# Kernel tuning notes

Hardware: AMD Instinct MI355X
Metric: run time of the kernel (lower is better)

The kernel has to match this reference:

```python
import jax, jax.numpy as jnp
import numpy as np

BS, N, HID, INPUT, PREK, KHOP = 16, 1024, 64, 64, 4, 3
D = 2 * HID            # hidden channel dim (128)
F = 2 * INPUT          # input feature dim (128)
C = F + D              # graphconv input channels (256)
NM = KHOP + 1          # num_metrics = k_hop*n_supports + 1 with n_supports=1
PI = 3.141592653589793
EMB_RANGE = (12.0 + 2.0) / HID   # (gamma + epsilon) / hidden_size


def setup_inputs() -> dict:
    key = jax.random.key(0)
    ks = jax.random.split(key, 12)
    inputs = jax.random.normal(ks[0], (BS, N, F), jnp.float32)
    # per-sample dynamic support; scale by 1/N to keep Chebyshev recursion stable
    supports = jax.random.uniform(ks[1], (BS, N, N), jnp.float32) / N
    hidden_states = jax.random.normal(ks[2], (BS, PREK, N, D), jnp.float32)
    W = jax.random.normal(ks[3], (D, D), jnp.float32) * 0.02
    b = jax.random.normal(ks[4], (N, D), jnp.float32) * 0.02
    R = jax.random.normal(ks[5], (PREK, N, HID), jnp.float32) * 0.02
    gc_w = jax.random.normal(ks[6], (D, C * NM), jnp.float32) * 0.02
    gc_b = jax.random.normal(ks[7], (D,), jnp.float32) * 0.02
    ev_att_w = jax.random.normal(ks[8], (1, N * D), jnp.float32) * 0.001
    ev_att_b = jax.random.normal(ks[9], (1,), jnp.float32) * 0.02
    att_w = jax.random.normal(ks[10], (1, N * D), jnp.float32) * 0.001
    att_b = jax.random.normal(ks[11], (1,), jnp.float32) * 0.02
    return {"inputs": inputs, "supports": supports, "hidden_states": hidden_states,
            "W": W, "b": b, "R": R, "gc_w": gc_w, "gc_b": gc_b,
            "ev_att_w": ev_att_w, "ev_att_b": ev_att_b,
            "att_w": att_w, "att_b": att_b}


def reference(inputs, supports, hidden_states, W, b, R, gc_w, gc_b,
              ev_att_w, ev_att_b, att_w, att_b):
    bs, k, n, d = hidden_states.shape
    # split inputs / last hidden into real/imag halves
    re_in, im_in = jnp.split(inputs, 2, axis=-1)          # [bs,n,INPUT]
    preH = hidden_states[:, -1]                           # [bs,n,d]
    re_p, im_p = jnp.split(preH, 2, axis=-1)              # [bs,n,HID]
    conv_in = jnp.concatenate([re_in, re_p, im_in, im_p], axis=-1)  # [bs,n,C]

    # diffusion graph conv (Chebyshev-style recursion over single batched support)
    x0 = conv_in
    x1 = jnp.matmul(supports, x0)                         # [bs,n,C]
    xs = [x0, x1]
    for _ in range(2, KHOP + 1):
        x2 = 2.0 * jnp.matmul(supports, x1) - x0
        xs.append(x2)
        x0, x1 = x1, x2
    # stack K metrics, permute to [bs,n,C,K], flatten (channel-major, step-minor)
    x = jnp.stack(xs, axis=0).transpose(1, 2, 3, 0).reshape(bs, n, C * NM)
    gco = x @ gc_w.T + gc_b                               # [bs,n,d]

    # EvolutionCell attention over g=1 group (kept for faithfulness)
    xe = gco.reshape(bs, 1, n * d)
    se = xe @ ev_att_w.T + ev_att_b                       # [bs,1,1]
    we = jax.nn.softmax(se, axis=1)
    conv_out = (xe * we).sum(axis=1).reshape(bs, n, d)

    # leaky_relu_ (slope 0.01)
    conv_out = jnp.where(conv_out >= 0, conv_out, 0.01 * conv_out)

    # RotatE-style complex phase rotation of hidden states
    phase = R / (EMB_RANGE / PI)                          # [k,n,HID]
    re_rel, im_rel = jnp.cos(phase), jnp.sin(phase)
    re_h, im_h = jnp.split(hidden_states, 2, axis=-1)     # [bs,k,n,HID]
    re_new = re_rel * re_h - im_rel * im_h
    im_new = im_rel * re_h + re_rel * im_h
    new_states = jnp.concatenate([re_new, im_new], axis=-1)  # [bs,k,n,d]

    # attention over k memory slots
    xa = new_states.reshape(bs, k, n * d)
    sa = xa @ att_w.T + att_b                             # [bs,k,1]
    wa = jax.nn.softmax(sa, axis=1)
    att = (xa * wa).sum(axis=1).reshape(bs, n, d)

    output = conv_out @ W + b[None] + att                 # [bs,n,d]
    new_hidden = jnp.concatenate([hidden_states[:, 1:], output[:, None]], axis=1)
    return output, new_hidden
```

## Files before the change

### kernel.cpp

```cpp
#include <hip/hip_runtime.h>
#include <cstddef>

constexpr float PHASE_SCALE = (float)(3.141592653589793 / ((12.0 + 2.0) / 64.0));

typedef __bf16 bf16;
typedef __bf16 bf16x4 __attribute__((ext_vector_type(4)));
typedef __bf16 bf16x8 __attribute__((ext_vector_type(8)));
typedef float floatx4 __attribute__((ext_vector_type(4)));

#define GLOAD_LDS16(gp, lp) __builtin_amdgcn_global_load_lds( \
    (const __attribute__((address_space(1))) void*)(gp),      \
    (__attribute__((address_space(3))) void*)(lp), 16, 0, 0)

__global__ __launch_bounds__(256) void prep_kernel(
    const float4* __restrict__ S, bf16* __restrict__ Sbf,
    const float* __restrict__ R,
    const float* __restrict__ gcw, const float* __restrict__ W,
    bf16* __restrict__ gtAll, bf16* __restrict__ WT,
    const float* __restrict__ inp, const float* __restrict__ hs,
    bf16* __restrict__ xRow, bf16* __restrict__ xT0,
    const float* __restrict__ attw, float* __restrict__ part)
{
    __shared__ bf16 tile[64][65];
    __shared__ float red[256];
    const int bid = blockIdx.x;
    const int tid = threadIdx.x;

    if (bid < 512) {
        int bk = bid & 63;
        int k = bk & 3;
        int chunk = bid >> 6;
        const float* hbase = hs + (size_t)bk * 131072;
        float acc = 0.f;
        for (int idx = tid; idx < 2048; idx += 256) {
            int h4 = (idx & 15) * 4;
            int n = chunk * 128 + (idx >> 4);
            float4 rr  = *(const float4*)(R + (size_t)k * 65536 + n * 64 + h4);
            float4 re  = *(const float4*)(hbase + (size_t)n * 128 + h4);
            float4 im  = *(const float4*)(hbase + (size_t)n * 128 + 64 + h4);
            float4 wre = *(const float4*)(attw + (size_t)n * 128 + h4);
            float4 wim = *(const float4*)(attw + (size_t)n * 128 + 64 + h4);
            float sv, cv;
            __sincosf(rr.x * PHASE_SCALE, &sv, &cv);
            acc += (cv * re.x - sv * im.x) * wre.x + (sv * re.x + cv * im.x) * wim.x;
            __sincosf(rr.y * PHASE_SCALE, &sv, &cv);
            acc += (cv * re.y - sv * im.y) * wre.y + (sv * re.y + cv * im.y) * wim.y;
            __sincosf(rr.z * PHASE_SCALE, &sv, &cv);
            acc += (cv * re.z - sv * im.z) * wre.z + (sv * re.z + cv * im.z) * wim.z;
            __sincosf(rr.w * PHASE_SCALE, &sv, &cv);
            acc += (cv * re.w - sv * im.w) * wre.w + (sv * re.w + cv * im.w) * wim.w;
        }
        red[tid] = acc;
        __syncthreads();
        for (int s2 = 128; s2 > 0; s2 >>= 1) {
            if (tid < s2) red[tid] += red[tid + s2];
            __syncthreads();
        }
        if (tid == 0) part[bk * 8 + chunk] = red[0];
    } else if (bid < 1536) {
        int lin = bid - 512;
        int b = lin >> 6, by = (lin >> 2) & 15, bx = lin & 3;
        int n0 = by * 64, c0 = bx * 64;
        const float* base = (bx & 1) ? (hs + (((size_t)b * 4 + 3) * 1024) * 128)
                                     : (inp + ((size_t)b * 1024) * 128);
        int soff = (bx >> 1) * 64;
        #pragma unroll
        for (int it = 0; it < 2; ++it) {
            int unit = it * 256 + tid;
            int nl = unit >> 3, cs = unit & 7;
            const float* src = base + (size_t)(n0 + nl) * 128 + soff + cs * 8;
            float4 a0 = *(const float4*)src;
            float4 a1 = *(const float4*)(src + 4);
            bf16x8 o;
            o[0] = (bf16)a0.x; o[1] = (bf16)a0.y; o[2] = (bf16)a0.z; o[3] = (bf16)a0.w;
            o[4] = (bf16)a1.x; o[5] = (bf16)a1.y; o[6] = (bf16)a1.z; o[7] = (bf16)a1.w;
            *(bf16x8*)(xRow + ((size_t)b * 1024 + n0 + nl) * 256 + c0 + cs * 8) = o;
            #pragma unroll
            for (int e = 0; e < 8; ++e) tile[nl][cs * 8 + e] = o[e];
        }
        __syncthreads();
        #pragma unroll
        for (int it = 0; it < 4; ++it) {
            int unit = it * 256 + tid;
            int ng = unit & 15, cc = unit >> 4;
            bf16x4 v;
            #pragma unroll
            for (int r = 0; r < 4; ++r) v[r] = tile[ng * 4 + r][cc];
            *(bf16x4*)(xT0 + ((size_t)b * 256 + c0 + cc) * 1024 + n0 + ng * 4) = v;
        }
    } else if (bid < 2112) {
        int gi = (bid - 1536) * 256 + tid;
        if (gi < 131072) {
            int m = gi >> 15;
            int rem = gi & 32767;
            int d = rem >> 8;
            int c = rem & 255;
            gtAll[gi] = (bf16)gcw[(size_t)d * 1024 + c * 4 + m];
        } else {
            int r = gi - 131072;
            int n = r >> 7, k = r & 127;
            WT[r] = (bf16)W[(size_t)k * 128 + n];
        }
    } else {
        size_t u = (size_t)(bid - 2112) * 512;
        #pragma unroll
        for (int i = 0; i < 2; ++i) {
            size_t gi = u + i * 256 + tid;
            const float4* Sp = S + gi * 2;
            float4 v0 = Sp[0];
            float4 v1 = Sp[1];
            bf16x8 o;
            o[0] = (bf16)v0.x; o[1] = (bf16)v0.y; o[2] = (bf16)v0.z; o[3] = (bf16)v0.w;
            o[4] = (bf16)v1.x; o[5] = (bf16)v1.y; o[6] = (bf16)v1.z; o[7] = (bf16)v1.w;
            *(bf16x8*)(Sbf + gi * 8) = o;
        }
    }
}

__global__ __launch_bounds__(512) void cheb_mfma_kernel(
    const bf16* __restrict__ S, const bf16* __restrict__ xT,
    const bf16* __restrict__ xTprev, bf16* __restrict__ outT,
    const bf16* __restrict__ xRow0, const bf16* __restrict__ gtA,
    const bf16* __restrict__ gt0, float* __restrict__ gcoF,
    float alpha, int accumulate)
{
    __shared__ char smem[81920];
    const int f = blockIdx.x;
    const int b = (f & 7) + 8 * ((f >> 3) & 1);
    const int n0 = (f >> 4) * 64;
    const int tid = threadIdx.x;
    const int wave = tid >> 6, lane = tid & 63;
    const int wr = (wave & 3) * 16;
    const int wc = (wave >> 2) * 128;
    const int l15 = lane & 15, quad = lane >> 4;
    const int lrow = lane >> 3;
    const int segsw = (lane & 7) ^ lrow;

    const bf16* Sb = S + (size_t)b * 1048576;
    const bf16* xb = xT + (size_t)b * 262144;

    auto stage = [&](int p, int k0) {
        bf16* dA = (bf16*)(smem + p * 40960);
        bf16* dB = dA + 4096;
        {
            const bf16* gp = Sb + (size_t)(n0 + wave * 8 + lrow) * 1024 + k0 + segsw * 8;
            GLOAD_LDS16(gp, dA + wave * 8 * 64);
        }
        #pragma unroll
        for (int v = 0; v < 4; ++v) {
            int cq = wave * 32 + v * 8;
            const bf16* gp = xb + (size_t)(cq + lrow) * 1024 + k0 + segsw * 8;
            GLOAD_LDS16(gp, dB + cq * 64);
        }
    };

    floatx4 acc[8] = {};
    stage(0, 0);
    int p = 0;
    for (int k0 = 0; k0 < 1024; k0 += 64) {
        __syncthreads();
        if (k0 + 64 < 1024) stage(p ^ 1, k0 + 64);
        const bf16* lA = (const bf16*)(smem + p * 40960);
        const bf16* lB = lA + 4096;
        #pragma unroll
        for (int ks = 0; ks < 2; ++ks) {
            int row = wr + l15;
            int aslot = (ks * 4 + quad) ^ (row & 7);
            bf16x8 af = *(const bf16x8*)(lA + row * 64 + aslot * 8);
            #pragma unroll
            for (int j = 0; j < 8; ++j) {
                int col = wc + j * 16 + l15;
                int bslot = (ks * 4 + quad) ^ (col & 7);
                bf16x8 bfr = *(const bf16x8*)(lB + col * 64 + bslot * 8);
                acc[j] = __builtin_amdgcn_mfma_f32_16x16x32_bf16(af, bfr, acc[j], 0, 0, 0);
            }
        }
        p ^= 1;
    }

    const bf16* pT = xTprev ? xTprev + (size_t)b * 262144 : nullptr;
    bf16* oT = outT ? outT + (size_t)b * 262144 : nullptr;
    bf16x4 xo[8];
    #pragma unroll
    for (int j = 0; j < 8; ++j) {
        int col = wc + j * 16 + l15;
        float v[4];
        #pragma unroll
        for (int r = 0; r < 4; ++r) v[r] = alpha * acc[j][r];
        if (pT) {
            bf16x4 pp = *(const bf16x4*)(pT + (size_t)col * 1024 + n0 + wr + quad * 4);
            #pragma unroll
            for (int r = 0; r < 4; ++r) v[r] -= (float)pp[r];
        }
        #pragma unroll
        for (int r = 0; r < 4; ++r) xo[j][r] = (bf16)v[r];
        if (oT) *(bf16x4*)(oT + (size_t)col * 1024 + n0 + wr + quad * 4) = xo[j];
    }

    __syncthreads();
    bf16* ldsX = (bf16*)smem;
    #pragma unroll
    for (int j = 0; j < 8; ++j) {
        int col = wc + j * 16 + l15;
        #pragma unroll
        for (int r = 0; r < 4; ++r)
            ldsX[(wr + quad * 4 + r) * 264 + col] = xo[j][r];
    }
    __syncthreads();

    const int dbase = (wave >> 2) * 64;
    floatx4 a2[4] = {};
    for (int k2 = 0; k2 < 256; k2 += 32) {
        bf16x8 af = *(const bf16x8*)(ldsX + (wr + l15) * 264 + k2 + quad * 8);
        #pragma unroll
        for (int j = 0; j < 4; ++j) {
            int dcol = dbase + j * 16 + l15;
            bf16x8 bfr = *(const bf16x8*)(gtA + (size_t)dcol * 256 + k2 + quad * 8);
            a2[j] = __builtin_amdgcn_mfma_f32_16x16x32_bf16(af, bfr, a2[j], 0, 0, 0);
        }
    }
    if (xRow0) {
        for (int k2 = 0; k2 < 256; k2 += 32) {
            bf16x8 af = *(const bf16x8*)(xRow0 + ((size_t)b * 1024 + n0 + wr + l15) * 256 + k2 + quad * 8);
            #pragma unroll
            for (int j = 0; j < 4; ++j) {
                int dcol = dbase + j * 16 + l15;
                bf16x8 bfr = *(const bf16x8*)(gt0 + (size_t)dcol * 256 + k2 + quad * 8);
                a2[j] = __builtin_amdgcn_mfma_f32_16x16x32_bf16(af, bfr, a2[j], 0, 0, 0);
            }
        }
    }
    #pragma unroll
    for (int j = 0; j < 4; ++j) {
        int dcol = dbase + j * 16 + l15;
        #pragma unroll
        for (int r = 0; r < 4; ++r) {
            size_t idx = ((size_t)b * 1024 + n0 + wr + quad * 4 + r) * 128 + dcol;
            if (accumulate) gcoF[idx] += a2[j][r];
            else            gcoF[idx]  = a2[j][r];
        }
    }
}

__global__ __launch_bounds__(256) void final_kernel(
    const float* __restrict__ gcoF, const float* __restrict__ gcb,
    const bf16* __restrict__ WT, const float* __restrict__ bvec,
    const float* __restrict__ hs, const float* __restrict__ R,
    const float* __restrict__ part, const float* __restrict__ attb,
    float* __restrict__ out, float* __restrict__ newh)
{
    const int m0 = blockIdx.x * 64;
    const int b = m0 >> 10, n0 = m0 & 1023;
    const int tid = threadIdx.x;
    const int wave = tid >> 6, lane = tid & 63;
    const int l15 = lane & 15, quad = lane >> 4;

    const int arow = m0 + wave * 16 + l15;
    floatx4 acc[8] = {};
    #pragma unroll
    for (int k0 = 0; k0 < 128; k0 += 32) {
        int kk = k0 + quad * 8;
        float4 p0 = *(const float4*)(gcoF + (size_t)arow * 128 + kk);
        float4 p1 = *(const float4*)(gcoF + (size_t)arow * 128 + kk + 4);
        float4 g0 = *(const float4*)(gcb + kk);
        float4 g1 = *(const float4*)(gcb + kk + 4);
        float vv[8] = {p0.x + g0.x, p0.y + g0.y, p0.z + g0.z, p0.w + g0.w,
                       p1.x + g1.x, p1.y + g1.y, p1.z + g1.z, p1.w + g1.w};
        bf16x8 af;
        #pragma unroll
        for (int e = 0; e < 8; ++e) {
            float v = vv[e];
            af[e] = (bf16)(v >= 0.f ? v : 0.01f * v);
        }
        #pragma unroll
        for (int j = 0; j < 8; ++j) {
            bf16x8 bfr = *(const bf16x8*)(WT + (size_t)(j * 16 + l15) * 128 + kk);
            acc[j] = __builtin_amdgcn_mfma_f32_16x16x32_bf16(af, bfr, acc[j], 0, 0, 0);
        }
    }

    float sa[4], mx = -1e30f;
    #pragma unroll
    for (int k = 0; k < 4; ++k) {
        float s = attb[0];
        #pragma unroll
        for (int c = 0; c < 8; ++c) s += part[(b * 4 + k) * 8 + c];
        sa[k] = s;
        mx = fmaxf(mx, s);
    }
    float den = 0.f;
    #pragma unroll
    for (int k = 0; k < 4; ++k) { sa[k] = __expf(sa[k] - mx); den += sa[k]; }
    float inv = 1.f / den;
    #pragma unroll
    for (int k = 0; k < 4; ++k) sa[k] *= inv;

    #pragma unroll
    for (int jj = 0; jj < 4; ++jj) {
        int hcol = jj * 16 + l15;
        #pragma unroll
        for (int r = 0; r < 4; ++r) {
            int n = n0 + wave * 16 + quad * 4 + r;
            float attRe = 0.f, attIm = 0.f;
            #pragma unroll
            for (int k = 0; k < 4; ++k) {
                const float* hb = hs + (((size_t)(b * 4 + k) * 1024 + n) * 128);
                float re = hb[hcol], im = hb[64 + hcol];
                float s, c;
                __sincosf(R[(size_t)k * 65536 + n * 64 + hcol] * PHASE_SCALE, &s, &c);
                attRe += sa[k] * (c * re - s * im);
                attIm += sa[k] * (s * re + c * im);
                if (k >= 1) {
                    size_t nb = (size_t)b * 524288 + (size_t)(k - 1) * 131072 + (size_t)n * 128;
                    newh[nb + hcol] = re;
                    newh[nb + 64 + hcol] = im;
                }
            }
            size_t ob = (size_t)(m0 + wave * 16 + quad * 4 + r) * 128;
            float oRe = acc[jj][r]     + bvec[(size_t)n * 128 + hcol]      + attRe;
            float oIm = acc[jj + 4][r] + bvec[(size_t)n * 128 + 64 + hcol] + attIm;
            out[ob + hcol] = oRe;
            out[ob + 64 + hcol] = oIm;
            size_t nb3 = (size_t)b * 524288 + 393216 + (size_t)n * 128;
            newh[nb3 + hcol] = oRe;
            newh[nb3 + 64 + hcol] = oIm;
        }
    }
}

extern "C" void kernel_launch(void* const* d_in, const int* in_sizes, int n_in,
                              void* d_out, int out_size, void* d_ws, size_t ws_size,
                              hipStream_t stream) {
    const float* inp  = (const float*)d_in[0];
    const float* sup  = (const float*)d_in[1];
    const float* hs   = (const float*)d_in[2];
    const float* W    = (const float*)d_in[3];
    const float* bvec = (const float*)d_in[4];
    const float* R    = (const float*)d_in[5];
    const float* gcw  = (const float*)d_in[6];
    const float* gcb  = (const float*)d_in[7];
    const float* attw = (const float*)d_in[10];
    const float* attb = (const float*)d_in[11];

    float* out  = (float*)d_out;
    float* newh = out + 2097152;
    bf16*  Sbf  = (bf16*)newh;

    char* w = (char*)d_ws;
    bf16*  xT0   = (bf16*)(w);
    bf16*  xT1   = (bf16*)(w + 8388608);
    bf16*  xT2   = (bf16*)(w + 16777216);
    bf16*  xRow  = (bf16*)(w + 25165824);
    float* gcoF  = (float*)(w + 33554432);
    bf16*  gtAll = (bf16*)(w + 41943040);
    bf16*  WT    = (bf16*)(w + 42205184);
    float* part  = (float*)(w + 42237952);

    prep_kernel<<<6208, 256, 0, stream>>>((const float4*)sup, Sbf, R, gcw, W,
                                          gtAll, WT, inp, hs, xRow, xT0, attw, part);

    cheb_mfma_kernel<<<256, 512, 0, stream>>>(Sbf, xT0, nullptr, xT1,
                                              xRow, gtAll + 32768, gtAll, gcoF, 1.0f, 0);
    cheb_mfma_kernel<<<256, 512, 0, stream>>>(Sbf, xT1, xT0, xT2,
                                              nullptr, gtAll + 2 * 32768, nullptr, gcoF, 2.0f, 1);
    cheb_mfma_kernel<<<256, 512, 0, stream>>>(Sbf, xT2, xT1, nullptr,
                                              nullptr, gtAll + 3 * 32768, nullptr, gcoF, 2.0f, 1);

    final_kernel<<<256, 256, 0, stream>>>(gcoF, gcb, WT, bvec, hs, R, part, attb, out, newh);
}
```

Before: 268.8 us.

## Triple-buffer Chebyshev MFMA K-loop with explicit vmcnt waits; rebalance prep grid

The Chebyshev MFMA kernel moves from a double-buffered to a triple-buffered LDS pipeline with a prefetch distance of two stages. It uses explicit s_waitcnt vmcnt counts and raw s_barrier instead of __syncthreads, so more global-to-LDS loads are in flight while MFMAs run. The prep kernel is reordered so the weight-transpose blocks come first, and the support fp32-to-bf16 conversion now does one 8-element chunk per thread across more blocks. In exchange, LDS per block grows to 120KB, and correctness depends on the hand-counted vmcnt matching the five loads issued per stage.

```diff
diff --git a/kernel.cpp b/kernel.cpp
--- a/kernel.cpp
+++ b/kernel.cpp
@@ -11,6 +11,8 @@
 #define GLOAD_LDS16(gp, lp) __builtin_amdgcn_global_load_lds( \
     (const __attribute__((address_space(1))) void*)(gp),      \
     (__attribute__((address_space(3))) void*)(lp), 16, 0, 0)
+
+#define VM_WAIT(n) asm volatile("s_waitcnt vmcnt(" #n ")" ::: "memory")
 
 __global__ __launch_bounds__(256) void prep_kernel(
     const float4* __restrict__ S, bf16* __restrict__ Sbf,
@@ -26,10 +28,24 @@
     const int bid = blockIdx.x;
     const int tid = threadIdx.x;
 
-    if (bid < 512) {
-        int bk = bid & 63;
+    if (bid < 576) {
+        int gi = bid * 256 + tid;
+        if (gi < 131072) {
+            int m = gi >> 15;
+            int rem = gi & 32767;
+            int d = rem >> 8;
+            int c = rem & 255;
+            gtAll[gi] = (bf16)gcw[(size_t)d * 1024 + c * 4 + m];
+        } else {
+            int r = gi - 131072;
+            int n = r >> 7, k = r & 127;
+            WT[r] = (bf16)W[(size_t)k * 128 + n];
+        }
+    } else if (bid < 1088) {
+        int bid3 = bid - 576;
+        int bk = bid3 & 63;
         int k = bk & 3;
-        int chunk = bid >> 6;
+        int chunk = bid3 >> 6;
         const float* hbase = hs + (size_t)bk * 131072;
         float acc = 0.f;
         for (int idx = tid; idx < 2048; idx += 256) {
@@ -57,8 +73,8 @@
             __syncthreads();
         }
         if (tid == 0) part[bk * 8 + chunk] = red[0];
-    } else if (bid < 1536) {
-        int lin = bid - 512;
+    } else if (bid < 2112) {
+        int lin = bid - 1088;
         int b = lin >> 6, by = (lin >> 2) & 15, bx = lin & 3;
         int n0 = by * 64, c0 = bx * 64;
         const float* base = (bx & 1) ? (hs + (((size_t)b * 4 + 3) * 1024) * 128)
@@ -88,32 +104,15 @@
             for (int r = 0; r < 4; ++r) v[r] = tile[ng * 4 + r][cc];
             *(bf16x4*)(xT0 + ((size_t)b * 256 + c0 + cc) * 1024 + n0 + ng * 4) = v;
         }
-    } else if (bid < 2112) {
-        int gi = (bid - 1536) * 256 + tid;
-        if (gi < 131072) {
-            int m = gi >> 15;
-            int rem = gi & 32767;
-            int d = rem >> 8;
-            int c = rem & 255;
-            gtAll[gi] = (bf16)gcw[(size_t)d * 1024 + c * 4 + m];
-        } else {
-            int r = gi - 131072;
-            int n = r >> 7, k = r & 127;
-            WT[r] = (bf16)W[(size_t)k * 128 + n];
-        }
     } else {
-        size_t u = (size_t)(bid - 2112) * 512;
-        #pragma unroll
-        for (int i = 0; i < 2; ++i) {
-            size_t gi = u + i * 256 + tid;
-            const float4* Sp = S + gi * 2;
-            float4 v0 = Sp[0];
-            float4 v1 = Sp[1];
-            bf16x8 o;
-            o[0] = (bf16)v0.x; o[1] = (bf16)v0.y; o[2] = (bf16)v0.z; o[3] = (bf16)v0.w;
-            o[4] = (bf16)v1.x; o[5] = (bf16)v1.y; o[6] = (bf16)v1.z; o[7] = (bf16)v1.w;
-            *(bf16x8*)(Sbf + gi * 8) = o;
-        }
+        int gi = (bid - 2112) * 256 + tid;
+        const float4* Sp = S + (size_t)gi * 2;
+        float4 v0 = Sp[0];
+        float4 v1 = Sp[1];
+        bf16x8 o;
+        o[0] = (bf16)v0.x; o[1] = (bf16)v0.y; o[2] = (bf16)v0.z; o[3] = (bf16)v0.w;
+        o[4] = (bf16)v1.x; o[5] = (bf16)v1.y; o[6] = (bf16)v1.z; o[7] = (bf16)v1.w;
+        *(bf16x8*)(Sbf + (size_t)gi * 8) = o;
     }
 }
 
@@ -124,7 +123,7 @@
     const bf16* __restrict__ gt0, float* __restrict__ gcoF,
     float alpha, int accumulate)
 {
-    __shared__ char smem[81920];
+    __shared__ char smem[122880];
     const int f = blockIdx.x;
     const int b = (f & 7) + 8 * ((f >> 3) & 1);
     const int n0 = (f >> 4) * 64;
@@ -139,8 +138,8 @@
     const bf16* Sb = S + (size_t)b * 1048576;
     const bf16* xb = xT + (size_t)b * 262144;
 
-    auto stage = [&](int p, int k0) {
-        bf16* dA = (bf16*)(smem + p * 40960);
+    auto stage = [&](int buf, int k0) {
+        bf16* dA = (bf16*)(smem + buf * 40960);
         bf16* dB = dA + 4096;
         {
             const bf16* gp = Sb + (size_t)(n0 + wave * 8 + lrow) * 1024 + k0 + segsw * 8;
@@ -156,11 +155,12 @@
 
     floatx4 acc[8] = {};
     stage(0, 0);
-    int p = 0;
-    for (int k0 = 0; k0 < 1024; k0 += 64) {
-        __syncthreads();
-        if (k0 + 64 < 1024) stage(p ^ 1, k0 + 64);
-        const bf16* lA = (const bf16*)(smem + p * 40960);
+    stage(1, 64);
+    for (int i = 0; i < 16; ++i) {
+        if (i < 15) { VM_WAIT(5); } else { VM_WAIT(0); }
+        __builtin_amdgcn_s_barrier();
+        __builtin_amdgcn_sched_barrier(0);
+        const bf16* lA = (const bf16*)(smem + (i % 3) * 40960);
         const bf16* lB = lA + 4096;
         #pragma unroll
         for (int ks = 0; ks < 2; ++ks) {
@@ -175,7 +175,7 @@
                 acc[j] = __builtin_amdgcn_mfma_f32_16x16x32_bf16(af, bfr, acc[j], 0, 0, 0);
             }
         }
-        p ^= 1;
+        if (i + 2 < 16) stage((i + 2) % 3, (i + 2) * 64);
     }
 
     const bf16* pT = xTprev ? xTprev + (size_t)b * 262144 : nullptr;
@@ -356,8 +356,8 @@
     bf16*  WT    = (bf16*)(w + 42205184);
     float* part  = (float*)(w + 42237952);
 
-    prep_kernel<<<6208, 256, 0, stream>>>((const float4*)sup, Sbf, R, gcw, W,
-                                          gtAll, WT, inp, hs, xRow, xT0, attw, part);
+    prep_kernel<<<10304, 256, 0, stream>>>((const float4*)sup, Sbf, R, gcw, W,
+                                           gtAll, WT, inp, hs, xRow, xT0, attw, part);
 
     cheb_mfma_kernel<<<256, 512, 0, stream>>>(Sbf, xT0, nullptr, xT1,
                                               xRow, gtAll + 32768, gtAll, gcoF, 1.0f, 0);
```

Result: faster. 262.8 us (-2.2%).
